# Performance work log

Measured on AMD Instinct MI355X. Metric: run time of the kernel, lower is better.

The kernel has to match this reference:

```python
import jax, jax.numpy as jnp
import numpy as np

NUM_BANKS = 32  # bank size (num_heads in __init__)
D_HEAD = 128
D_MODEL = 2048
B, S, K = 2, 1024, 4  # batch, seq, selected heads per token


def setup_inputs() -> dict:
    key = jax.random.key(0)
    k1, k2, k3, k4, k5 = jax.random.split(key, 5)
    tensor = jax.random.normal(k1, (B, S, K, D_HEAD), dtype=jnp.float32)
    head_selection = jax.random.randint(k2, (B, S, K), 0, NUM_BANKS)
    head_probabilities = jax.random.uniform(k3, (B, S, K), dtype=jnp.float32)
    # Banked linear parameters: one (d_head, d_model) matrix + bias per bank.
    W = jax.random.normal(k4, (NUM_BANKS, D_HEAD, D_MODEL), dtype=jnp.float32) * (1.0 / np.sqrt(D_HEAD))
    b = jax.random.normal(k5, (NUM_BANKS, D_MODEL), dtype=jnp.float32) * 0.01
    return {"tensor": tensor, "head_selection": head_selection,
            "head_probabilities": head_probabilities, "W": W, "b": b}


def reference(tensor, head_selection, head_probabilities, W, b):
    # BankedLinear: per (token, head-slot) select weight matrix W[sel] and
    # compute x @ W[sel] + b[sel] -> (..., k, d_model).
    # Implemented as a one-hot dispatch so the contraction is a single
    # grouped-GEMM-shaped einsum instead of materializing an
    # (B,S,K,d_head,d_model) gathered weight tensor.
    onehot = jax.nn.one_hot(head_selection, NUM_BANKS, dtype=tensor.dtype)  # (B,S,K,N)
    proj = jnp.einsum('bskd,bskn,ndm->bskm', tensor, onehot, W)             # (B,S,K,d_model)
    proj = proj + jnp.einsum('bskn,nm->bskm', onehot, b)                    # gathered bias
    # Head merge: matmul(proj^T, probs.unsqueeze(-1)).squeeze(-1)
    # == probability-weighted sum over the head dimension.
    out = jnp.einsum('bskm,bsk->bsm', proj, head_probabilities)             # (B,S,d_model)
    return out
```

## Files before the change

### kernel.cpp

```cpp
#include <hip/hip_runtime.h>
#include <hip/hip_bf16.h>

#define NBANK 32
#define DHEAD 128
#define DMODEL 2048
#define NSLOT 8192
#define NTOK 2048
#define XCROWS 1024

typedef __attribute__((ext_vector_type(8))) short short8;
typedef __attribute__((ext_vector_type(8))) float float8;
typedef __attribute__((ext_vector_type(4))) float f32x4;

__device__ __forceinline__ unsigned short f2bf(float f) {
    union { __hip_bfloat16 h; unsigned short u; } cvt;
    cvt.h = __float2bfloat16(f);
    return cvt.u;
}
__device__ __forceinline__ float bf2f(unsigned short u) {
    union { float f; unsigned int v; } cvt;
    cvt.v = ((unsigned int)u) << 16;
    return cvt.f;
}

__global__ void convW_kernel(const float* __restrict__ W,
                             unsigned short* __restrict__ wfrag) {
    int t = blockIdx.x * 256 + threadIdx.x;
    int lane = t & 63;
    int kk = (t >> 6) & 3;
    int mt = (t >> 8) & 127;
    int bank = t >> 15;
    int m = mt * 16 + (lane & 15);
    int kbase = kk * 32 + (lane >> 4) * 8;
    const float* src = W + ((size_t)bank * DHEAD + kbase) * DMODEL + m;
    short8 o;
    #pragma unroll
    for (int v = 0; v < 8; ++v)
        o[v] = (short)f2bf(src[v * DMODEL]);
    reinterpret_cast<short8*>(wfrag)[t] = o;
}

__global__ void bucket_kernel(const int* __restrict__ sel,
                              int* __restrict__ counts,
                              int* __restrict__ lists) {
    __shared__ int lcount[NBANK];
    __shared__ int lbase[NBANK];
    int tid = threadIdx.x;
    int slot = blockIdx.x * 256 + tid;
    if (tid < NBANK) lcount[tid] = 0;
    __syncthreads();
    int bank = sel[slot];
    int mypos = atomicAdd(&lcount[bank], 1);
    __syncthreads();
    if (tid < NBANK) lbase[tid] = atomicAdd(&counts[tid], lcount[tid]);
    __syncthreads();
    lists[bank * NSLOT + lbase[bank] + mypos] = slot;
}

__global__ void compact_kernel(const float* __restrict__ x,
                               const float* __restrict__ probs,
                               const int* __restrict__ counts,
                               const int* __restrict__ lists,
                               unsigned short* __restrict__ xc) {
    int bank = blockIdx.x;
    int wv = (threadIdx.x >> 6) + blockIdx.y * 4;
    int lane = threadIdx.x & 63;
    int cnt = counts[bank];
    for (int pos = wv; pos < cnt; pos += 16) {
        int slot = lists[bank * NSLOT + pos];
        float p = probs[slot];
        float2 v = reinterpret_cast<const float2*>(x + (size_t)slot * DHEAD)[lane];
        ushort2 o;
        o.x = f2bf(v.x * p);
        o.y = f2bf(v.y * p);
        reinterpret_cast<ushort2*>(xc + ((size_t)bank * XCROWS + pos) * DHEAD)[lane] = o;
    }
}

__global__ __launch_bounds__(256, 4)
void gemm_kernel(const unsigned short* __restrict__ wfrag,
                 const unsigned short* __restrict__ xc,
                 const int* __restrict__ counts,
                 const int* __restrict__ lists,
                 unsigned short* __restrict__ proj) {
    __shared__ __align__(16) unsigned short A_lds[16 * DHEAD];
    __shared__ int slots_lds[16];

    int tid = threadIdx.x;
    int w = tid >> 6;
    int lane = tid & 63;
    int lane_lo = lane & 15;
    int lane_hi = lane >> 4;
    int bank = blockIdx.y;
    int mw = blockIdx.x * 256 + w * 64;
    int mt0 = mw >> 4;
    int cnt = counts[bank];

    const short8* wf = reinterpret_cast<const short8*>(wfrag);
    short8 bw[4][4];
    #pragma unroll
    for (int nf = 0; nf < 4; ++nf)
        #pragma unroll
        for (int kk = 0; kk < 4; ++kk)
            bw[kk][nf] = wf[((((bank * 128 + mt0 + nf) * 4) + kk) << 6) + lane];

    int row16 = tid >> 4, j = tid & 15;
    const char* xc_b = reinterpret_cast<const char*>(xc)
                     + ((size_t)bank * XCROWS + row16) * 256
                     + ((j ^ (row16 & 7)) << 4);
    char* lds_b = reinterpret_cast<char*>(A_lds);
    char* lds_dst = lds_b + (w << 10);

    for (int rt = blockIdx.z; rt * 16 < cnt; rt += 4) {
        __syncthreads();
        __builtin_amdgcn_global_load_lds(
            (const __attribute__((address_space(1))) void*)(xc_b + (size_t)rt * 16 * 256),
            (__attribute__((address_space(3))) void*)lds_dst, 16, 0, 0);
        if (tid < 16) {
            int ridx = rt * 16 + tid;
            slots_lds[tid] = (ridx < cnt) ? lists[bank * NSLOT + ridx] : -1;
        }
        __syncthreads();

        f32x4 acc[4] = {{0.f,0.f,0.f,0.f},{0.f,0.f,0.f,0.f},
                        {0.f,0.f,0.f,0.f},{0.f,0.f,0.f,0.f}};
        #pragma unroll
        for (int kk = 0; kk < 4; ++kk) {
            int byteoff = lane_lo * 256 +
                          ((kk * 64 + lane_hi * 16) ^ ((lane_lo & 7) << 4));
            short8 a = *reinterpret_cast<const short8*>(lds_b + byteoff);
            #pragma unroll
            for (int nf = 0; nf < 4; ++nf)
                acc[nf] = __builtin_amdgcn_mfma_f32_16x16x32_bf16(
                              a, bw[kk][nf], acc[nf], 0, 0, 0);
        }

        #pragma unroll
        for (int v = 0; v < 4; ++v) {
            int row = lane_hi * 4 + v;
            int slot = slots_lds[row];
            if (slot >= 0) {
                unsigned short* pr = proj + (size_t)slot * DMODEL + mw + lane_lo;
                #pragma unroll
                for (int nf = 0; nf < 4; ++nf)
                    pr[nf * 16] = f2bf(acc[nf][v]);
            }
        }
    }
}

__global__ void merge_kernel(const unsigned short* __restrict__ proj,
                             const int* __restrict__ sel,
                             const float* __restrict__ probs,
                             const float* __restrict__ bias,
                             float* __restrict__ out) {
    int tid = threadIdx.x;
    int tok = blockIdx.x;
    float8 acc = {0.f, 0.f, 0.f, 0.f, 0.f, 0.f, 0.f, 0.f};
    #pragma unroll
    for (int k = 0; k < 4; ++k) {
        int slot = tok * 4 + k;
        short8 pr = reinterpret_cast<const short8*>(proj + (size_t)slot * DMODEL)[tid];
        float p = probs[slot];
        int bk = sel[slot];
        float8 bv = reinterpret_cast<const float8*>(bias + (size_t)bk * DMODEL)[tid];
        #pragma unroll
        for (int jj = 0; jj < 8; ++jj)
            acc[jj] += bf2f((unsigned short)pr[jj]) + p * bv[jj];
    }
    reinterpret_cast<float8*>(out + (size_t)tok * DMODEL)[tid] = acc;
}

extern "C" void kernel_launch(void* const* d_in, const int* in_sizes, int n_in,
                              void* d_out, int out_size, void* d_ws, size_t ws_size,
                              hipStream_t stream) {
    const float* x     = (const float*)d_in[0];
    const int*   sel   = (const int*)  d_in[1];
    const float* probs = (const float*)d_in[2];
    const float* W     = (const float*)d_in[3];
    const float* bias  = (const float*)d_in[4];
    float* out = (float*)d_out;

    char* ws = (char*)d_ws;
    int* counts = (int*)ws;
    int* lists  = (int*)(ws + 1024);
    unsigned short* xc    = (unsigned short*)(ws + (2u  << 20));
    unsigned short* wfrag = (unsigned short*)(ws + (12u << 20));
    unsigned short* proj  = (unsigned short*)(ws + (32u << 20));

    hipMemsetAsync(counts, 0, 128, stream);
    convW_kernel<<<4096, 256, 0, stream>>>(W, wfrag);
    bucket_kernel<<<32, 256, 0, stream>>>(sel, counts, lists);
    compact_kernel<<<dim3(32, 4), 256, 0, stream>>>(x, probs, counts, lists, xc);
    gemm_kernel<<<dim3(8, 32, 4), 256, 0, stream>>>(wfrag, xc, counts, lists, proj);
    merge_kernel<<<2048, 256, 0, stream>>>(proj, sel, probs, bias, out);
}
```

Measured before the change: 132.6 us.

## Fuse weight conversion with bucketing and retile grouped GEMM per wave

Merges the weight-conversion and bank-bucketing kernels into a single launch, with block index deciding the role, to drop one launch and its serialization gap. The GEMM now gives each wave 32 output columns instead of 64 and splits rows across 2 z-slices instead of 4. That halves the B-fragment register footprint per wave and changes how many blocks reuse each loaded A tile. Counts are clamped to XCROWS as a safety bound, and the xc buffer offset moves so it no longer overlaps the enlarged list region.

```diff
diff --git a/kernel.cpp b/kernel.cpp
--- a/kernel.cpp
+++ b/kernel.cpp
@@ -7,6 +7,7 @@
 #define NSLOT 8192
 #define NTOK 2048
 #define XCROWS 1024
+#define CONV_BLOCKS 4096
 
 typedef __attribute__((ext_vector_type(8))) short short8;
 typedef __attribute__((ext_vector_type(8))) float float8;
@@ -23,38 +24,39 @@
     return cvt.f;
 }
 
-__global__ void convW_kernel(const float* __restrict__ W,
-                             unsigned short* __restrict__ wfrag) {
-    int t = blockIdx.x * 256 + threadIdx.x;
-    int lane = t & 63;
-    int kk = (t >> 6) & 3;
-    int mt = (t >> 8) & 127;
-    int bank = t >> 15;
-    int m = mt * 16 + (lane & 15);
-    int kbase = kk * 32 + (lane >> 4) * 8;
-    const float* src = W + ((size_t)bank * DHEAD + kbase) * DMODEL + m;
-    short8 o;
-    #pragma unroll
-    for (int v = 0; v < 8; ++v)
-        o[v] = (short)f2bf(src[v * DMODEL]);
-    reinterpret_cast<short8*>(wfrag)[t] = o;
-}
-
-__global__ void bucket_kernel(const int* __restrict__ sel,
-                              int* __restrict__ counts,
-                              int* __restrict__ lists) {
-    __shared__ int lcount[NBANK];
-    __shared__ int lbase[NBANK];
-    int tid = threadIdx.x;
-    int slot = blockIdx.x * 256 + tid;
-    if (tid < NBANK) lcount[tid] = 0;
-    __syncthreads();
-    int bank = sel[slot];
-    int mypos = atomicAdd(&lcount[bank], 1);
-    __syncthreads();
-    if (tid < NBANK) lbase[tid] = atomicAdd(&counts[tid], lcount[tid]);
-    __syncthreads();
-    lists[bank * NSLOT + lbase[bank] + mypos] = slot;
+__global__ void prep_kernel(const float* __restrict__ W,
+                            unsigned short* __restrict__ wfrag,
+                            const int* __restrict__ sel,
+                            int* __restrict__ counts,
+                            int* __restrict__ lists) {
+    if (blockIdx.x < CONV_BLOCKS) {
+        int t = blockIdx.x * 256 + threadIdx.x;
+        int lane = t & 63;
+        int kk = (t >> 6) & 3;
+        int mt = (t >> 8) & 127;
+        int bank = t >> 15;
+        int m = mt * 16 + (lane & 15);
+        int kbase = kk * 32 + (lane >> 4) * 8;
+        const float* src = W + ((size_t)bank * DHEAD + kbase) * DMODEL + m;
+        short8 o;
+        #pragma unroll
+        for (int v = 0; v < 8; ++v)
+            o[v] = (short)f2bf(src[v * DMODEL]);
+        reinterpret_cast<short8*>(wfrag)[t] = o;
+    } else {
+        __shared__ int lcount[NBANK];
+        __shared__ int lbase[NBANK];
+        int tid = threadIdx.x;
+        int slot = (blockIdx.x - CONV_BLOCKS) * 256 + tid;
+        if (tid < NBANK) lcount[tid] = 0;
+        __syncthreads();
+        int bank = sel[slot];
+        int mypos = atomicAdd(&lcount[bank], 1);
+        __syncthreads();
+        if (tid < NBANK) lbase[tid] = atomicAdd(&counts[tid], lcount[tid]);
+        __syncthreads();
+        lists[bank * NSLOT + lbase[bank] + mypos] = slot;
+    }
 }
 
 __global__ void compact_kernel(const float* __restrict__ x,
@@ -65,7 +67,7 @@
     int bank = blockIdx.x;
     int wv = (threadIdx.x >> 6) + blockIdx.y * 4;
     int lane = threadIdx.x & 63;
-    int cnt = counts[bank];
+    int cnt = min(counts[bank], XCROWS);
     for (int pos = wv; pos < cnt; pos += 16) {
         int slot = lists[bank * NSLOT + pos];
         float p = probs[slot];
@@ -92,14 +94,14 @@
     int lane_lo = lane & 15;
     int lane_hi = lane >> 4;
     int bank = blockIdx.y;
-    int mw = blockIdx.x * 256 + w * 64;
+    int mw = blockIdx.x * 128 + w * 32;
     int mt0 = mw >> 4;
-    int cnt = counts[bank];
+    int cnt = min(counts[bank], XCROWS);
 
     const short8* wf = reinterpret_cast<const short8*>(wfrag);
-    short8 bw[4][4];
+    short8 bw[4][2];
     #pragma unroll
-    for (int nf = 0; nf < 4; ++nf)
+    for (int nf = 0; nf < 2; ++nf)
         #pragma unroll
         for (int kk = 0; kk < 4; ++kk)
             bw[kk][nf] = wf[((((bank * 128 + mt0 + nf) * 4) + kk) << 6) + lane];
@@ -111,10 +113,10 @@
     char* lds_b = reinterpret_cast<char*>(A_lds);
     char* lds_dst = lds_b + (w << 10);
 
-    for (int rt = blockIdx.z; rt * 16 < cnt; rt += 4) {
+    for (int rt = blockIdx.z; rt * 16 < cnt; rt += 2) {
         __syncthreads();
         __builtin_amdgcn_global_load_lds(
-            (const __attribute__((address_space(1))) void*)(xc_b + (size_t)rt * 16 * 256),
+            (const __attribute__((address_space(1))) void*)(xc_b + (size_t)rt * 4096),
             (__attribute__((address_space(3))) void*)lds_dst, 16, 0, 0);
         if (tid < 16) {
             int ridx = rt * 16 + tid;
@@ -122,17 +124,15 @@
         }
         __syncthreads();
 
-        f32x4 acc[4] = {{0.f,0.f,0.f,0.f},{0.f,0.f,0.f,0.f},
-                        {0.f,0.f,0.f,0.f},{0.f,0.f,0.f,0.f}};
+        f32x4 acc0 = {0.f, 0.f, 0.f, 0.f};
+        f32x4 acc1 = {0.f, 0.f, 0.f, 0.f};
         #pragma unroll
         for (int kk = 0; kk < 4; ++kk) {
             int byteoff = lane_lo * 256 +
                           ((kk * 64 + lane_hi * 16) ^ ((lane_lo & 7) << 4));
             short8 a = *reinterpret_cast<const short8*>(lds_b + byteoff);
-            #pragma unroll
-            for (int nf = 0; nf < 4; ++nf)
-                acc[nf] = __builtin_amdgcn_mfma_f32_16x16x32_bf16(
-                              a, bw[kk][nf], acc[nf], 0, 0, 0);
+            acc0 = __builtin_amdgcn_mfma_f32_16x16x32_bf16(a, bw[kk][0], acc0, 0, 0, 0);
+            acc1 = __builtin_amdgcn_mfma_f32_16x16x32_bf16(a, bw[kk][1], acc1, 0, 0, 0);
         }
 
         #pragma unroll
@@ -141,9 +141,8 @@
             int slot = slots_lds[row];
             if (slot >= 0) {
                 unsigned short* pr = proj + (size_t)slot * DMODEL + mw + lane_lo;
-                #pragma unroll
-                for (int nf = 0; nf < 4; ++nf)
-                    pr[nf * 16] = f2bf(acc[nf][v]);
+                pr[0]  = f2bf(acc0[v]);
+                pr[16] = f2bf(acc1[v]);
             }
         }
     }
@@ -184,14 +183,13 @@
     char* ws = (char*)d_ws;
     int* counts = (int*)ws;
     int* lists  = (int*)(ws + 1024);
-    unsigned short* xc    = (unsigned short*)(ws + (2u  << 20));
+    unsigned short* xc    = (unsigned short*)(ws + (3u  << 20));
     unsigned short* wfrag = (unsigned short*)(ws + (12u << 20));
     unsigned short* proj  = (unsigned short*)(ws + (32u << 20));
 
     hipMemsetAsync(counts, 0, 128, stream);
-    convW_kernel<<<4096, 256, 0, stream>>>(W, wfrag);
-    bucket_kernel<<<32, 256, 0, stream>>>(sel, counts, lists);
+    prep_kernel<<<CONV_BLOCKS + 32, 256, 0, stream>>>(W, wfrag, sel, counts, lists);
     compact_kernel<<<dim3(32, 4), 256, 0, stream>>>(x, probs, counts, lists, xc);
-    gemm_kernel<<<dim3(8, 32, 4), 256, 0, stream>>>(wfrag, xc, counts, lists, proj);
+    gemm_kernel<<<dim3(16, 32, 2), 256, 0, stream>>>(wfrag, xc, counts, lists, proj);
     merge_kernel<<<2048, 256, 0, stream>>>(proj, sel, probs, bias, out);
 }
```

New measurement: 128.7 us. -2.9%, faster.
